# Kernel optimization log

Measured on AMD Instinct MI355X. Metric: run time of the kernel, lower is better.

Reference implementation:

```python
import jax, jax.numpy as jnp
import numpy as np

# --- config constants (from init_kwargs) ---
ALPHA = 0.05; SIGMA = 0.2; THETA = 0.3; A = 0.02; B_PAR = 0.1; RHO = 0.5
MULT = 2.0          # config.x_range_final[1]
GAMMA = 0.5         # power-utility exponent: u(x,r)=r*x^g/g, ux=r*x^(g-1)
N_STEPS = 100; T_FINAL = 1.0; DT = T_FINAL / N_STEPS
HID = 64; BATCH = 16384
PEN_SCALE = 100.0; LOWER = 1e-6


def _mlp(W1, b1, W2, b2, W3, b3, s):
    # tiny FeedForwardSubNet: 3 -> HID -> HID -> 1, tanh activations
    h = jnp.tanh(s @ W1 + b1)
    h = jnp.tanh(h @ W2 + b2)
    return h @ W3 + b3


def _penalise(v):
    # penalise_range(v, lower): quadratic hinge below `lower`
    return PEN_SCALE * jnp.square(jnp.maximum(LOWER - v, 0.0))


def setup_inputs() -> dict:
    key = jax.random.key(0)
    ks = jax.random.split(key, 16)
    dw = jax.random.normal(ks[0], (BATCH, 1, N_STEPS), dtype=jnp.float32) * float(np.sqrt(DT))
    X0 = jnp.ones((1,), jnp.float32)
    R0 = jnp.ones((1,), jnp.float32)
    def w(k, shape, fan):
        return jax.random.normal(k, shape, jnp.float32) / np.float32(np.sqrt(fan))
    inp = {"dw": dw, "X0": X0, "R0": R0,
           "pW1": w(ks[1], (3, HID), 3), "pb1": jnp.zeros((HID,), jnp.float32),
           "pW2": w(ks[2], (HID, HID), HID), "pb2": jnp.zeros((HID,), jnp.float32),
           "pW3": w(ks[3], (HID, 1), HID), "pb3": jnp.zeros((1,), jnp.float32),
           "qW1": w(ks[4], (3, HID), 3), "qb1": jnp.zeros((HID,), jnp.float32),
           "qW2": w(ks[5], (HID, HID), HID), "qb2": jnp.zeros((HID,), jnp.float32),
           "qW3": w(ks[6], (HID, 1), HID), "qb3": jnp.zeros((1,), jnp.float32)}
    return inp


def reference(dw, X0, R0, pW1, pb1, pW2, pb2, pW3, pb3, qW1, qb1, qW2, qb2, qW3, qb3):
    Bn = dw.shape[0]
    ones = jnp.ones((Bn, 1), dw.dtype)
    times = jnp.arange(N_STEPS + 1, dtype=dw.dtype) * DT   # [N+1]
    x0 = ones * X0
    R0v = ones * R0
    b_eff = float(np.sign(RHO)) * B_PAR

    # p_0 and dp_0 = d p_0 / d x (per-sample, rowwise independent net)
    def p_of_x(xx):
        st = jnp.concatenate([MULT * times[0] * ones, xx, R0v], 1)
        return _mlp(pW1, pb1, pW2, pb2, pW3, pb3, st)
    p0, p_vjp = jax.vjp(p_of_x, x0)
    (dp0,) = p_vjp(jnp.ones_like(p0))
    pi0 = _mlp(qW1, qb1, qW2, qb2, qW3, qb3,
               jnp.concatenate([MULT * times[0] * ones, x0, R0v], 1))

    dw_t = jnp.transpose(dw, (2, 0, 1))          # [N, B, 1]
    upd = jnp.arange(N_STEPS) < (N_STEPS - 1)    # pi not updated at last step

    def step(carry, inp):
        x, min_x, W, pi = carry
        dwi, t_next, u = inp
        x = x + x * ALPHA * DT + pi * SIGMA * THETA * DT + pi * SIGMA * dwi
        min_x = jnp.minimum(x, min_x)
        W = W + dwi
        Rv = R0v * jnp.exp((A - 0.5 * b_eff ** 2) * t_next + b_eff * W)
        p = p0 * jnp.exp(-(ALPHA + 0.5 * THETA ** 2) * t_next - THETA * W)
        st = jnp.concatenate([MULT * t_next * jnp.ones_like(x), x, Rv], 1)
        pi_new = _mlp(qW1, qb1, qW2, qb2, qW3, qb3, st)
        pi = jnp.where(u, pi_new, pi)
        return (x, min_x, W, pi), (x, Rv, pi, -p)

    (xf, min_x, Wf, pif), (xs, Rs, pis, dMs) = jax.lax.scan(
        step, (x0, x0, jnp.zeros_like(x0), pi0), (dw_t, times[1:], upd))

    # stacked process data, matching tf.concat-over-axis-0 ordering: [(N+1)*B, 1]
    x_all  = jnp.concatenate([x0[None], xs], 0).reshape(-1, 1)
    r_all  = jnp.concatenate([R0v[None], Rs], 0).reshape(-1, 1)
    pi_all = jnp.concatenate([pi0[None], pis], 0).reshape(-1, 1)
    dM_all = jnp.concatenate([(-p0)[None], dMs], 0).reshape(-1, 1)
    dM2_all = jnp.tile(-dp0, (N_STEPS + 1, 1))
    proc = jnp.concatenate([x_all, r_all, pi_all, dM_all, dM2_all], 1)  # [(N+1)*B, 5]

    # losses (non_concave = False branch)
    p_fin = -dMs[-1]
    R_fin = Rs[-1]
    xc = jnp.maximum(xf, LOWER)
    ux = R_fin * xc ** (GAMMA - 1.0)
    u_val = R_fin * xc ** GAMMA / GAMMA
    pen = _penalise(min_x)
    loss_p = jnp.mean(jnp.square(p_fin + ux) + pen)
    loss_pi = loss_p + jnp.mean(-u_val + pen)

    return jnp.concatenate([proc.reshape(-1), jnp.stack([loss_p, loss_pi])])
```

## Files before the change

kernel.cpp:

```cpp
#include <hip/hip_runtime.h>
#include <hip/hip_bf16.h>
#include <math.h>

#define NSTEP 100
#define BATCH 16384
#define MB 16
#define NBLK (BATCH/MB)
#define NT 128

#define C_ALPHA 0.05f
#define C_SIGMA 0.2f
#define C_THETA 0.3f
#define C_DT    0.01f
#define C_LOWER 1e-6f
#define C_PEN   100.0f
#define LOG2E   1.4426950408889634f
#define TSCALE  (2.0f * LOG2E)
#define CRT ( 0.015f * C_DT * LOG2E)
#define CRW ( 0.1f * LOG2E)
#define CPT (-0.095f * C_DT * LOG2E)
#define CPW (-0.3f * LOG2E)

#define WG_BARRIER() asm volatile("s_waitcnt lgkmcnt(0)\n\ts_barrier" ::: "memory")

typedef __attribute__((ext_vector_type(8))) short bf16x8;
typedef __attribute__((ext_vector_type(4))) float f32x4;
typedef __attribute__((ext_vector_type(4), aligned(4))) float f32x4a;

__device__ __forceinline__ float tanh_pre(float zs) {
    float e = __builtin_amdgcn_exp2f(zs);
    return 1.0f - 2.0f * __builtin_amdgcn_rcpf(e + 1.0f);
}
__device__ __forceinline__ unsigned f2bf_u(float f) {
    unsigned u = __float_as_uint(f);
    return (u + 0x7FFFu + ((u >> 16) & 1u)) >> 16;
}
__device__ __forceinline__ unsigned pack_bf16(float a, float b) {
    union { __hip_bfloat162 h; unsigned u; } cv;
    cv.h = __float22bfloat162_rn(make_float2(a, b));
    return cv.u;
}
__device__ __forceinline__ float dpp_row_sum16(float v) {
    int t;
    t = __builtin_amdgcn_update_dpp(0, __float_as_int(v), 0x128, 0xF, 0xF, true);
    v += __int_as_float(t);
    t = __builtin_amdgcn_update_dpp(0, __float_as_int(v), 0x124, 0xF, 0xF, true);
    v += __int_as_float(t);
    t = __builtin_amdgcn_update_dpp(0, __float_as_int(v), 0x122, 0xF, 0xF, true);
    v += __int_as_float(t);
    t = __builtin_amdgcn_update_dpp(0, __float_as_int(v), 0x121, 0xF, 0xF, true);
    v += __int_as_float(t);
    return v;
}

__global__ __launch_bounds__(NT, 2) void fused_kernel(
        const float* __restrict__ dw, const float* __restrict__ X0,
        const float* __restrict__ R0,
        const float* __restrict__ pW1, const float* __restrict__ pb1,
        const float* __restrict__ pW2, const float* __restrict__ pb2,
        const float* __restrict__ pW3, const float* __restrict__ pb3,
        const float* __restrict__ qW1, const float* __restrict__ qb1,
        const float* __restrict__ qW2, const float* __restrict__ qb2,
        const float* __restrict__ qW3, const float* __restrict__ qb3,
        float* __restrict__ ws, float* __restrict__ out) {
    __shared__ __align__(16) unsigned short sW2T[64 * 72];
    __shared__ __align__(16) float sdw[MB * NSTEP];
    __shared__ __align__(16) uint4 sA[2][2][64];
    __shared__ __align__(16) float sP[2][2][16];

    const int tid = threadIdx.x;
    const int lane = tid & 63;
    const int wv = tid >> 6;
    const int b0 = blockIdx.x * MB;
    const int l15 = lane & 15, quad = lane >> 4;

    {
        const float4* g = (const float4*)(dw + (size_t)b0 * NSTEP);
        float4* s = (float4*)sdw;
        #pragma unroll
        for (int u = tid; u < MB * NSTEP / 4; u += NT) s[u] = g[u];
    }
    for (int u = tid; u < 4096; u += NT) {
        int k = u >> 6, n = u & 63;
        sW2T[n * 72 + k] = (unsigned short)f2bf_u(qW2[u] * TSCALE);
    }
    __syncthreads();

    bf16x8 Bf[2][2];
    #pragma unroll
    for (int t = 0; t < 2; t++) {
        const unsigned short* r = &sW2T[(wv * 32 + t * 16 + l15) * 72 + quad * 8];
        Bf[t][0] = *(const bf16x8*)r;
        Bf[t][1] = *(const bf16x8*)(r + 32);
    }
    float tco[8], w1xs[8], w1rs[8], b1s[8];
    #pragma unroll
    for (int j = 0; j < 8; j++) {
        int k = wv * 32 + quad * 8 + j;
        tco[j]  = qW1[k] * (2.0f * C_DT * TSCALE);
        w1xs[j] = qW1[64 + k] * TSCALE;
        w1rs[j] = qW1[128 + k] * TSCALE;
        b1s[j]  = qb1[k] * TSCALE;
    }
    float b2v[2], w3v[2];
    #pragma unroll
    for (int t = 0; t < 2; t++) {
        b2v[t] = qb2[wv * 32 + t * 16 + l15] * TSCALE;
        w3v[t] = qW3[wv * 32 + t * 16 + l15];
    }
    const float b3 = qb3[0];
    const float X0v = X0[0], R0s = R0[0];

    float p0, dp0;
    {
        float pre = fmaf(pW1[64 + lane], X0v, fmaf(pW1[128 + lane], R0s, pb1[lane]));
        float h1 = tanh_pre(TSCALE * pre);
        float d1 = (1.0f - h1 * h1) * pW1[64 + lane];
        float a0 = pb2[lane], a1 = 0.f, a2 = 0.f, a3 = 0.f;
        float e0 = 0.f, e1 = 0.f, e2 = 0.f, e3 = 0.f;
        for (int i2 = 0; i2 < 64; i2 += 4) {
            float w0 = pW2[(i2 + 0) * 64 + lane];
            float w1 = pW2[(i2 + 1) * 64 + lane];
            float w2 = pW2[(i2 + 2) * 64 + lane];
            float w3 = pW2[(i2 + 3) * 64 + lane];
            a0 = fmaf(__shfl(h1, i2 + 0), w0, a0); e0 = fmaf(__shfl(d1, i2 + 0), w0, e0);
            a1 = fmaf(__shfl(h1, i2 + 1), w1, a1); e1 = fmaf(__shfl(d1, i2 + 1), w1, e1);
            a2 = fmaf(__shfl(h1, i2 + 2), w2, a2); e2 = fmaf(__shfl(d1, i2 + 2), w2, e2);
            a3 = fmaf(__shfl(h1, i2 + 3), w3, a3); e3 = fmaf(__shfl(d1, i2 + 3), w3, e3);
        }
        float pre2 = (a0 + a1) + (a2 + a3);
        float dpre2 = (e0 + e1) + (e2 + e3);
        float h2 = tanh_pre(TSCALE * pre2);
        float d2 = (1.0f - h2 * h2) * dpre2;
        float c1 = h2 * pW3[lane], c2 = d2 * pW3[lane];
        #pragma unroll
        for (int o = 1; o < 64; o <<= 1) {
            c1 += __shfl_xor(c1, o);
            c2 += __shfl_xor(c2, o);
        }
        p0 = c1 + pb3[0]; dp0 = c2;
    }
    const float mdp0 = -dp0;

    auto qnet = [&](int par, float fi, float xv, float rv) -> float {
        union { uint4 u4; bf16x8 v; unsigned u[4]; } Aloc, Aoth;
        #pragma unroll
        for (int p = 0; p < 4; p++) {
            const int i0 = 2 * p, i1 = 2 * p + 1;
            float z0 = fmaf(w1rs[i0], rv, fmaf(w1xs[i0], xv, fmaf(tco[i0], fi, b1s[i0])));
            float z1 = fmaf(w1rs[i1], rv, fmaf(w1xs[i1], xv, fmaf(tco[i1], fi, b1s[i1])));
            Aloc.u[p] = pack_bf16(tanh_pre(z0), tanh_pre(z1));
        }
        sA[par][wv][lane] = Aloc.u4;
        WG_BARRIER();
        Aoth.u4 = sA[par][1 - wv][lane];
        bf16x8 A0 = (wv == 0) ? Aloc.v : Aoth.v;
        bf16x8 A1 = (wv == 0) ? Aoth.v : Aloc.v;
        f32x4 acc0 = {b2v[0], b2v[0], b2v[0], b2v[0]};
        f32x4 acc1 = {b2v[1], b2v[1], b2v[1], b2v[1]};
        acc0 = __builtin_amdgcn_mfma_f32_16x16x32_bf16(A0, Bf[0][0], acc0, 0, 0, 0);
        acc1 = __builtin_amdgcn_mfma_f32_16x16x32_bf16(A0, Bf[1][0], acc1, 0, 0, 0);
        acc0 = __builtin_amdgcn_mfma_f32_16x16x32_bf16(A1, Bf[0][1], acc0, 0, 0, 0);
        acc1 = __builtin_amdgcn_mfma_f32_16x16x32_bf16(A1, Bf[1][1], acc1, 0, 0, 0);
        f32x4 part;
        #pragma unroll
        for (int r = 0; r < 4; r++)
            part[r] = dpp_row_sum16(
                fmaf(tanh_pre(acc1[r]), w3v[1], tanh_pre(acc0[r]) * w3v[0]));
        if (l15 == 0) *(f32x4*)&sP[par][wv][quad * 4] = part;
        WG_BARRIER();
        return sP[par][0][l15] + sP[par][1][l15] + b3;
    };

    float x = X0v, Wsum = 0.0f, minx = X0v;
    float pi = qnet(0, 0.0f, X0v, R0s);
    if (wv == 1) {
        size_t base = (size_t)(b0 + l15) * 5;
        if (quad == 0) {
            f32x4a o = {X0v, R0s, pi, -p0};
            *(f32x4a*)(out + base) = o;
        } else if (quad == 1) {
            out[base + 4] = mdp0;
        }
    }

    float dw_next = sdw[l15 * NSTEP];
    #pragma unroll 2
    for (int i = 0; i < NSTEP - 1; i++) {
        const float fi = (float)(i + 1);
        float dwv = dw_next;
        dw_next = sdw[l15 * NSTEP + i + 1];
        float t = pi * C_SIGMA;
        x = fmaf(x, 1.0f + C_ALPHA * C_DT, fmaf(t, dwv, t * (C_THETA * C_DT)));
        minx = fminf(minx, x);
        Wsum += dwv;
        float R = R0s * __builtin_amdgcn_exp2f(fmaf(CRW, Wsum, CRT * fi));
        float pm = p0 * __builtin_amdgcn_exp2f(fmaf(CPW, Wsum, CPT * fi));
        float pin = qnet((i + 1) & 1, fi, x, R);
        if (wv == 1) {
            size_t base = ((size_t)(i + 1) * BATCH + b0 + l15) * 5;
            if (quad == 0) {
                f32x4a o = {x, R, pin, -pm};
                *(f32x4a*)(out + base) = o;
            } else if (quad == 1) {
                out[base + 4] = mdp0;
            }
        }
        pi = pin;
    }

    {
        float dwv = dw_next;
        float t = pi * C_SIGMA;
        x = fmaf(x, 1.0f + C_ALPHA * C_DT, fmaf(t, dwv, t * (C_THETA * C_DT)));
        minx = fminf(minx, x);
        Wsum += dwv;
        float Rf = R0s * __builtin_amdgcn_exp2f(fmaf(CRW, Wsum, CRT * (float)NSTEP));
        float pf = p0 * __builtin_amdgcn_exp2f(fmaf(CPW, Wsum, CPT * (float)NSTEP));
        if (wv == 1) {
            size_t base = ((size_t)NSTEP * BATCH + b0 + l15) * 5;
            if (quad == 0) {
                f32x4a o = {x, Rf, pi, -pf};
                *(f32x4a*)(out + base) = o;
            } else if (quad == 1) {
                out[base + 4] = mdp0;
            }
        }
        if (wv == 0) {
            float xc = fmaxf(x, C_LOWER);
            float ux = Rf * rsqrtf(xc);
            float uval = 2.0f * Rf * sqrtf(xc);
            float d = fmaxf(C_LOWER - minx, 0.0f);
            float pen = C_PEN * d * d;
            float t1 = pf + ux;
            float v1 = dpp_row_sum16(t1 * t1 + pen);
            float v2 = dpp_row_sum16(-uval + pen);
            if (lane == 0) {
                atomicAdd(&ws[3], v1);
                atomicAdd(&ws[4], v2);
                __threadfence();
                int old = atomicAdd((int*)(ws + 5), 1);
                if (old == NBLK - 1) {
                    float lp = atomicAdd(&ws[3], 0.0f) * (1.0f / (float)BATCH);
                    float lq = atomicAdd(&ws[4], 0.0f) * (1.0f / (float)BATCH);
                    out[(size_t)(NSTEP + 1) * BATCH * 5] = lp;
                    out[(size_t)(NSTEP + 1) * BATCH * 5 + 1] = lp + lq;
                }
            }
        }
    }
}

extern "C" void kernel_launch(void* const* d_in, const int* in_sizes, int n_in,
                              void* d_out, int out_size, void* d_ws, size_t ws_size,
                              hipStream_t stream) {
    const float* dw  = (const float*)d_in[0];
    const float* X0  = (const float*)d_in[1];
    const float* R0  = (const float*)d_in[2];
    const float* pW1 = (const float*)d_in[3];
    const float* pb1 = (const float*)d_in[4];
    const float* pW2 = (const float*)d_in[5];
    const float* pb2 = (const float*)d_in[6];
    const float* pW3 = (const float*)d_in[7];
    const float* pb3 = (const float*)d_in[8];
    const float* qW1 = (const float*)d_in[9];
    const float* qb1 = (const float*)d_in[10];
    const float* qW2 = (const float*)d_in[11];
    const float* qb2 = (const float*)d_in[12];
    const float* qW3 = (const float*)d_in[13];
    const float* qb3 = (const float*)d_in[14];
    float* out = (float*)d_out;
    float* ws  = (float*)d_ws;

    hipMemsetAsync(d_ws, 0, 64, stream);
    fused_kernel<<<NBLK, NT, 0, stream>>>(dw, X0, R0, pW1, pb1, pW2, pb2, pW3, pb3,
                                          qW1, qb1, qW2, qb2, qW3, qb3, ws, out);
}
```

Measured before the change: 206.4 us.

## Split per-block q-net work across four waves instead of two

Doubles threads per block to 256 so each wave computes one 16-column slice of the second layer and a quarter of the first-layer activations. Per-wave serial tanh and MFMA work per time step shrinks, which shortens the sequential 100-step dependency chain. In exchange, cross-wave reductions now combine four partial sums, and barriers synchronise more waves. The loop is no longer unrolled and the pm exponential is computed only in the writing wave.

```diff
diff --git a/kernel.cpp b/kernel.cpp
--- a/kernel.cpp
+++ b/kernel.cpp
@@ -6,7 +6,7 @@
 #define BATCH 16384
 #define MB 16
 #define NBLK (BATCH/MB)
-#define NT 128
+#define NT 256
 
 #define C_ALPHA 0.05f
 #define C_SIGMA 0.2f
@@ -53,7 +53,7 @@
     return v;
 }
 
-__global__ __launch_bounds__(NT, 2) void fused_kernel(
+__global__ __launch_bounds__(NT, 4) void fused_kernel(
         const float* __restrict__ dw, const float* __restrict__ X0,
         const float* __restrict__ R0,
         const float* __restrict__ pW1, const float* __restrict__ pb1,
@@ -65,19 +65,20 @@
         float* __restrict__ ws, float* __restrict__ out) {
     __shared__ __align__(16) unsigned short sW2T[64 * 72];
     __shared__ __align__(16) float sdw[MB * NSTEP];
-    __shared__ __align__(16) uint4 sA[2][2][64];
-    __shared__ __align__(16) float sP[2][2][16];
+    __shared__ __align__(16) uint2 sA2[2][2][64][2];
+    __shared__ __align__(16) float sP[2][4][16];
 
     const int tid = threadIdx.x;
     const int lane = tid & 63;
     const int wv = tid >> 6;
+    const int ks_own = wv >> 1;
+    const int half = wv & 1;
     const int b0 = blockIdx.x * MB;
     const int l15 = lane & 15, quad = lane >> 4;
 
     {
         const float4* g = (const float4*)(dw + (size_t)b0 * NSTEP);
         float4* s = (float4*)sdw;
-        #pragma unroll
         for (int u = tid; u < MB * NSTEP / 4; u += NT) s[u] = g[u];
     }
     for (int u = tid; u < 4096; u += NT) {
@@ -86,28 +87,25 @@
     }
     __syncthreads();
 
-    bf16x8 Bf[2][2];
-    #pragma unroll
-    for (int t = 0; t < 2; t++) {
-        const unsigned short* r = &sW2T[(wv * 32 + t * 16 + l15) * 72 + quad * 8];
-        Bf[t][0] = *(const bf16x8*)r;
-        Bf[t][1] = *(const bf16x8*)(r + 32);
-    }
-    float tco[8], w1xs[8], w1rs[8], b1s[8];
-    #pragma unroll
-    for (int j = 0; j < 8; j++) {
-        int k = wv * 32 + quad * 8 + j;
-        tco[j]  = qW1[k] * (2.0f * C_DT * TSCALE);
-        w1xs[j] = qW1[64 + k] * TSCALE;
-        w1rs[j] = qW1[128 + k] * TSCALE;
-        b1s[j]  = qb1[k] * TSCALE;
-    }
-    float b2v[2], w3v[2];
-    #pragma unroll
-    for (int t = 0; t < 2; t++) {
-        b2v[t] = qb2[wv * 32 + t * 16 + l15] * TSCALE;
-        w3v[t] = qW3[wv * 32 + t * 16 + l15];
-    }
+    bf16x8 Bf0, Bf1;
+    {
+        const unsigned short* r = &sW2T[(wv * 16 + l15) * 72 + quad * 8];
+        Bf0 = *(const bf16x8*)r;
+        Bf1 = *(const bf16x8*)(r + 32);
+    }
+    float tco[4], w1xs[4], w1rs[4], b1s[4];
+    {
+        const int kb = ks_own * 32 + quad * 8 + half * 4;
+        #pragma unroll
+        for (int j = 0; j < 4; j++) {
+            tco[j]  = qW1[kb + j] * (2.0f * C_DT * TSCALE);
+            w1xs[j] = qW1[64 + kb + j] * TSCALE;
+            w1rs[j] = qW1[128 + kb + j] * TSCALE;
+            b1s[j]  = qb1[kb + j] * TSCALE;
+        }
+    }
+    const float b2v = qb2[wv * 16 + l15] * TSCALE;
+    const float w3v = qW3[wv * 16 + l15];
     const float b3 = qb3[0];
     const float X0v = X0[0], R0s = R0[0];
 
@@ -143,38 +141,35 @@
     const float mdp0 = -dp0;
 
     auto qnet = [&](int par, float fi, float xv, float rv) -> float {
-        union { uint4 u4; bf16x8 v; unsigned u[4]; } Aloc, Aoth;
-        #pragma unroll
-        for (int p = 0; p < 4; p++) {
-            const int i0 = 2 * p, i1 = 2 * p + 1;
-            float z0 = fmaf(w1rs[i0], rv, fmaf(w1xs[i0], xv, fmaf(tco[i0], fi, b1s[i0])));
-            float z1 = fmaf(w1rs[i1], rv, fmaf(w1xs[i1], xv, fmaf(tco[i1], fi, b1s[i1])));
-            Aloc.u[p] = pack_bf16(tanh_pre(z0), tanh_pre(z1));
-        }
-        sA[par][wv][lane] = Aloc.u4;
+        union { uint2 u2; unsigned u[2]; } Aloc;
+        {
+            float z0 = fmaf(w1rs[0], rv, fmaf(w1xs[0], xv, fmaf(tco[0], fi, b1s[0])));
+            float z1 = fmaf(w1rs[1], rv, fmaf(w1xs[1], xv, fmaf(tco[1], fi, b1s[1])));
+            float z2 = fmaf(w1rs[2], rv, fmaf(w1xs[2], xv, fmaf(tco[2], fi, b1s[2])));
+            float z3 = fmaf(w1rs[3], rv, fmaf(w1xs[3], xv, fmaf(tco[3], fi, b1s[3])));
+            Aloc.u[0] = pack_bf16(tanh_pre(z0), tanh_pre(z1));
+            Aloc.u[1] = pack_bf16(tanh_pre(z2), tanh_pre(z3));
+        }
+        sA2[par][ks_own][lane][half] = Aloc.u2;
         WG_BARRIER();
-        Aoth.u4 = sA[par][1 - wv][lane];
-        bf16x8 A0 = (wv == 0) ? Aloc.v : Aoth.v;
-        bf16x8 A1 = (wv == 0) ? Aoth.v : Aloc.v;
-        f32x4 acc0 = {b2v[0], b2v[0], b2v[0], b2v[0]};
-        f32x4 acc1 = {b2v[1], b2v[1], b2v[1], b2v[1]};
-        acc0 = __builtin_amdgcn_mfma_f32_16x16x32_bf16(A0, Bf[0][0], acc0, 0, 0, 0);
-        acc1 = __builtin_amdgcn_mfma_f32_16x16x32_bf16(A0, Bf[1][0], acc1, 0, 0, 0);
-        acc0 = __builtin_amdgcn_mfma_f32_16x16x32_bf16(A1, Bf[0][1], acc0, 0, 0, 0);
-        acc1 = __builtin_amdgcn_mfma_f32_16x16x32_bf16(A1, Bf[1][1], acc1, 0, 0, 0);
+        bf16x8 A0 = *(const bf16x8*)&sA2[par][0][lane][0];
+        bf16x8 A1 = *(const bf16x8*)&sA2[par][1][lane][0];
+        f32x4 acc = {b2v, b2v, b2v, b2v};
+        acc = __builtin_amdgcn_mfma_f32_16x16x32_bf16(A0, Bf0, acc, 0, 0, 0);
+        acc = __builtin_amdgcn_mfma_f32_16x16x32_bf16(A1, Bf1, acc, 0, 0, 0);
         f32x4 part;
         #pragma unroll
         for (int r = 0; r < 4; r++)
-            part[r] = dpp_row_sum16(
-                fmaf(tanh_pre(acc1[r]), w3v[1], tanh_pre(acc0[r]) * w3v[0]));
+            part[r] = dpp_row_sum16(tanh_pre(acc[r]) * w3v);
         if (l15 == 0) *(f32x4*)&sP[par][wv][quad * 4] = part;
         WG_BARRIER();
-        return sP[par][0][l15] + sP[par][1][l15] + b3;
+        return ((sP[par][0][l15] + sP[par][1][l15]) +
+                (sP[par][2][l15] + sP[par][3][l15])) + b3;
     };
 
     float x = X0v, Wsum = 0.0f, minx = X0v;
     float pi = qnet(0, 0.0f, X0v, R0s);
-    if (wv == 1) {
+    if (wv == 3) {
         size_t base = (size_t)(b0 + l15) * 5;
         if (quad == 0) {
             f32x4a o = {X0v, R0s, pi, -p0};
@@ -185,7 +180,7 @@
     }
 
     float dw_next = sdw[l15 * NSTEP];
-    #pragma unroll 2
+    #pragma unroll 1
     for (int i = 0; i < NSTEP - 1; i++) {
         const float fi = (float)(i + 1);
         float dwv = dw_next;
@@ -195,9 +190,9 @@
         minx = fminf(minx, x);
         Wsum += dwv;
         float R = R0s * __builtin_amdgcn_exp2f(fmaf(CRW, Wsum, CRT * fi));
-        float pm = p0 * __builtin_amdgcn_exp2f(fmaf(CPW, Wsum, CPT * fi));
         float pin = qnet((i + 1) & 1, fi, x, R);
-        if (wv == 1) {
+        if (wv == 3) {
+            float pm = p0 * __builtin_amdgcn_exp2f(fmaf(CPW, Wsum, CPT * fi));
             size_t base = ((size_t)(i + 1) * BATCH + b0 + l15) * 5;
             if (quad == 0) {
                 f32x4a o = {x, R, pin, -pm};
@@ -217,7 +212,7 @@
         Wsum += dwv;
         float Rf = R0s * __builtin_amdgcn_exp2f(fmaf(CRW, Wsum, CRT * (float)NSTEP));
         float pf = p0 * __builtin_amdgcn_exp2f(fmaf(CPW, Wsum, CPT * (float)NSTEP));
-        if (wv == 1) {
+        if (wv == 3) {
             size_t base = ((size_t)NSTEP * BATCH + b0 + l15) * 5;
             if (quad == 0) {
                 f32x4a o = {x, Rf, pi, -pf};
```

Result: no change. 205.6 us (-0.4%).
